# Kernel tuning notes

Measured on AMD Instinct MI355X. Metric: run time of the kernel, lower is better.

Reference implementation:

```python
import jax, jax.numpy as jnp
import numpy as np

NUM_QUBITS = 12
NUM_LAYERS = 4
N_CLASSES = 10
BATCH = 512
BN_EPS = 1e-5


def _apply_1q(state, U, wire):
    """Apply a 1-qubit gate U on `wire`. state: (B,)+(2,)*n; U: (2,2) or (B,2,2)."""
    state = jnp.moveaxis(state, wire + 1, -1)
    if U.ndim == 3:
        out = jnp.einsum('bij,b...j->b...i', U, state)
    else:
        out = jnp.einsum('ij,b...j->b...i', U, state)
    return jnp.moveaxis(out, -1, wire + 1)


def _apply_cnot(state, ctrl, tgt):
    s = jnp.moveaxis(state, (ctrl + 1, tgt + 1), (-2, -1))
    # where control bit == 1, flip the target axis
    s = jnp.concatenate([s[..., 0:1, :], s[..., 1:2, ::-1]], axis=-2)
    return jnp.moveaxis(s, (-2, -1), (ctrl + 1, tgt + 1))


def _rot(phi, theta, omega):
    """PennyLane Rot(phi, theta, omega) = RZ(omega) RY(theta) RZ(phi)."""
    c = jnp.cos(theta / 2)
    s = jnp.sin(theta / 2)
    row0 = jnp.stack([jnp.exp(-1j * (phi + omega) / 2) * c,
                      -jnp.exp(1j * (phi - omega) / 2) * s])
    row1 = jnp.stack([jnp.exp(-1j * (phi - omega) / 2) * s,
                      jnp.exp(1j * (phi + omega) / 2) * c])
    return jnp.stack([row0, row1]).astype(jnp.complex64)


def _circuit(x, weights):
    """Batched state-vector sim of the data-reuploading VQC.
    x: (B, n_qubits) angles; weights: (L, n_qubits, 3). Returns (B, N_CLASSES) <Z_i>."""
    B = x.shape[0]
    state = jnp.zeros((B,) + (2,) * NUM_QUBITS, jnp.complex64)
    state = state.at[(slice(None),) + (0,) * NUM_QUBITS].set(1.0)
    half = (x * 0.5).astype(jnp.float32)
    for l in range(NUM_LAYERS):
        w = weights[l]
        # angle embedding (RY(x_q) on each wire) -- batched gate, differs per sample
        for q in range(NUM_QUBITS):
            c = jnp.cos(half[:, q])
            s = jnp.sin(half[:, q])
            U = jnp.stack([jnp.stack([c, -s], -1),
                           jnp.stack([s, c], -1)], -2).astype(jnp.complex64)  # (B,2,2)
            state = _apply_1q(state, U, q)
        # one StronglyEntangling layer: Rot per wire (shared across batch)
        for q in range(NUM_QUBITS):
            state = _apply_1q(state, _rot(w[q, 0], w[q, 1], w[q, 2]), q)
        # ring of CNOTs (range 1)
        for q in range(NUM_QUBITS):
            state = _apply_cnot(state, q, (q + 1) % NUM_QUBITS)
    probs = jnp.abs(state) ** 2  # (B,)+(2,)*n, float32
    all_axes = tuple(range(1, NUM_QUBITS + 1))
    expz = []
    for i in range(N_CLASSES):
        axes = tuple(a for a in all_axes if a != i + 1)
        p = probs.sum(axis=axes)  # (B, 2) marginal of qubit i
        expz.append(p[:, 0] - p[:, 1])
    return jnp.stack(expz, axis=-1)  # (B, N_CLASSES)


def setup_inputs() -> dict:
    key = jax.random.key(0)
    k1, k2 = jax.random.split(key)
    x = jax.random.normal(k1, (BATCH, NUM_QUBITS), dtype=jnp.float32)
    weights = 0.01 * jax.random.uniform(k2, (NUM_LAYERS, NUM_QUBITS, 3), dtype=jnp.float32)
    bias = jnp.zeros((N_CLASSES,), jnp.float32)
    gamma = jnp.ones((N_CLASSES,), jnp.float32)
    beta = jnp.zeros((N_CLASSES,), jnp.float32)
    return {"x": x, "weights": weights, "bias": bias, "gamma": gamma, "beta": beta}


def reference(x, weights, bias, gamma, beta):
    expz = _circuit(x, weights)
    probs = jax.nn.softmax(expz + bias, axis=-1)
    # BatchNorm1d (training mode): biased batch statistics, affine
    mu = probs.mean(axis=0)
    var = probs.var(axis=0)
    return (probs - mu) / jnp.sqrt(var + BN_EPS) * gamma + beta
```

## Files before the change

kernel.cpp:

```cpp
#include <hip/hip_runtime.h>
#include <math.h>

#define NQ 12
#define NL 4
#define NC 10
#define NB 512
#define BN_EPS 1e-5f

typedef float v2f __attribute__((ext_vector_type(2)));

__device__ __forceinline__ void bfly(v2f& A, v2f& B,
    v2f c0, v2f c1, v2f c2, v2f c3, v2f c4, v2f c5, v2f c6, v2f c7)
{
    const v2f As = A.yx, Bs = B.yx;
    const v2f An = __builtin_elementwise_fma(c0, A,
                   __builtin_elementwise_fma(c1, As,
                   __builtin_elementwise_fma(c2, B, c3 * Bs)));
    const v2f Bn = __builtin_elementwise_fma(c4, A,
                   __builtin_elementwise_fma(c5, As,
                   __builtin_elementwise_fma(c6, B, c7 * Bs)));
    A = An; B = Bn;
}

__global__ __launch_bounds__(512, 4) void vqc_kernel(
    const float* __restrict__ x, const float* __restrict__ w,
    const float* __restrict__ bias, float* __restrict__ probs)
{
    __shared__ v2f buf[2][4096];
    __shared__ __align__(16) float gm[48][16];
    __shared__ float red[8*NC];

    const int b = blockIdx.x;
    const int t = threadIdx.x;

    if (t < 48) {
        const int l = t / NQ, q = t % NQ;
        const float xq = 0.5f * x[b*NQ + q];
        const float cx = cosf(xq), sx = sinf(xq);
        const int wi = (l*NQ + q)*3;
        const float phi = w[wi], tht = w[wi+1], om = w[wi+2];
        const float ct = cosf(0.5f*tht), st = sinf(0.5f*tht);
        const float aa = 0.5f*(phi + om), dd = 0.5f*(phi - om);
        const float ca = cosf(aa), sa = sinf(aa);
        const float cd = cosf(dd), sd = sinf(dd);
        const float u00r =  ca*ct, u00i = -sa*ct;
        const float u01r = -cd*st, u01i = -sd*st;
        const float u10r =  cd*st, u10i = -sd*st;
        const float u11r =  ca*ct, u11i =  sa*ct;
        const float m00r = u00r*cx + u01r*sx, m00i = u00i*cx + u01i*sx;
        const float m01r = u01r*cx - u00r*sx, m01i = u01i*cx - u00i*sx;
        const float m10r = u10r*cx + u11r*sx, m10i = u10i*cx + u11i*sx;
        const float m11r = u11r*cx - u10r*sx, m11i = u11i*cx - u10i*sx;
        float* gp = gm[t];
        gp[0]  =  m00r; gp[1]  = m00r;
        gp[2]  = -m00i; gp[3]  = m00i;
        gp[4]  =  m01r; gp[5]  = m01r;
        gp[6]  = -m01i; gp[7]  = m01i;
        gp[8]  =  m10r; gp[9]  = m10r;
        gp[10] = -m10i; gp[11] = m10i;
        gp[12] =  m11r; gp[13] = m11r;
        gp[14] = -m11i; gp[15] = m11i;
    }
    __syncthreads();

    v2f a[8];
    #pragma unroll
    for (int r = 0; r < 8; ++r) a[r] = (v2f){0.f, 0.f};
    if (t == 0) a[0].x = 1.f;

    const unsigned tu = (unsigned)t;
    const unsigned tw = tu >> 6;
    const unsigned baseB = (tw << 9) | (tu & 63u);
    const unsigned baseC = (tw << 9) | (((tu >> 3) & 7u) << 6) | (tu & 7u);
    const unsigned baseD = (tw << 9) | (((tu >> 3) & 7u) << 6) | ((tu & 7u) << 3);

#define SWZ(i) ((i) ^ (((i) >> 4) & 15u))

    #define STAGE(gbase) \
        _Pragma("unroll") \
        for (int g = 0; g < 3; ++g) { \
            const v2f* cp = (const v2f*)gm[(gbase) + 2 - g]; \
            const v2f c0=cp[0],c1=cp[1],c2=cp[2],c3=cp[3], \
                      c4=cp[4],c5=cp[5],c6=cp[6],c7=cp[7]; \
            const int bit = 1 << g; \
            _Pragma("unroll") \
            for (int r0 = 0; r0 < 8; ++r0) \
                if (!(r0 & bit)) bfly(a[r0], a[r0|bit], c0,c1,c2,c3,c4,c5,c6,c7); \
        }

    #define TRANS(IOLD, INEW) { \
        v2f* bp = buf[pb]; pb ^= 1; \
        _Pragma("unroll") \
        for (int r = 0; r < 8; ++r) { const unsigned i_ = (IOLD); bp[SWZ(i_)] = a[r]; } \
        __syncthreads(); \
        _Pragma("unroll") \
        for (int r = 0; r < 8; ++r) { const unsigned i_ = (INEW); a[r] = bp[SWZ(i_)]; } \
    }

    int pb = 0;
    #pragma unroll
    for (int l = 0; l < NL; ++l) {
        STAGE(l*12)
        TRANS(((unsigned)r << 9) | tu, baseB | ((unsigned)r << 6))
        STAGE(l*12 + 3)
        TRANS(baseB | ((unsigned)r << 6), baseC | ((unsigned)r << 3))
        STAGE(l*12 + 6)
        TRANS(baseC | ((unsigned)r << 3), baseD | (unsigned)r)
        STAGE(l*12 + 9)
        if (l < NL-1) {
            v2f* bp = buf[pb]; pb ^= 1;
            #pragma unroll
            for (int r = 0; r < 8; ++r) {
                unsigned i_ = baseD | (unsigned)r;
                unsigned S = i_ ^ (i_ >> 1);
                S ^= S >> 2; S ^= S >> 4; S ^= S >> 8;
                const unsigned j = S ^ ((S & 1u) << 11);
                bp[SWZ(j)] = a[r];
            }
            __syncthreads();
            #pragma unroll
            for (int r = 0; r < 8; ++r) {
                const unsigned i_ = ((unsigned)r << 9) | tu;
                a[r] = bp[SWZ(i_)];
            }
        }
    }

    const unsigned t8 = (tu >> 8) & 1u;
    const unsigned Q7 = t8 ^ ((tu >> 7) & 1u);
    const unsigned Q6 = Q7 ^ ((tu >> 6) & 1u);
    const unsigned Q5 = Q6 ^ ((tu >> 5) & 1u);
    const unsigned Q4 = Q5 ^ ((tu >> 4) & 1u);
    const unsigned Q3 = Q4 ^ ((tu >> 3) & 1u);
    const unsigned Q2 = Q3 ^ ((tu >> 2) & 1u);
    const unsigned Q1 = Q2 ^ ((tu >> 1) & 1u);
    const unsigned Q0 = Q1 ^ (tu & 1u);

    float psum = 0.f, pflip = 0.f, pflip2 = 0.f;
    #pragma unroll
    for (int r = 0; r < 8; ++r) {
        const float p = a[r].x*a[r].x + a[r].y*a[r].y;
        const int pr = ((r>>2) ^ (r>>1) ^ r) & 1;
        psum  += p;
        pflip  += pr      ? -p : p;
        pflip2 += (r & 4) ? -p : p;
    }
    float acc[NC];
    acc[0] = ((t8 ^ Q0) ? -1.f : 1.f) * pflip;
    acc[1] = (Q7 ? -1.f : 1.f) * psum;
    acc[2] = (Q6 ? -1.f : 1.f) * psum;
    acc[3] = (Q5 ? -1.f : 1.f) * psum;
    acc[4] = (Q4 ? -1.f : 1.f) * psum;
    acc[5] = (Q3 ? -1.f : 1.f) * psum;
    acc[6] = (Q2 ? -1.f : 1.f) * psum;
    acc[7] = (Q1 ? -1.f : 1.f) * psum;
    acc[8] = (Q0 ? -1.f : 1.f) * psum;
    acc[9] = (Q0 ? -1.f : 1.f) * pflip2;

    #pragma unroll
    for (int off = 32; off >= 1; off >>= 1) {
        #pragma unroll
        for (int c = 0; c < NC; ++c)
            acc[c] += __shfl_down(acc[c], off, 64);
    }
    const int wave = t >> 6, lane = t & 63;
    if (lane == 0) {
        #pragma unroll
        for (int c = 0; c < NC; ++c) red[wave*NC + c] = acc[c];
    }
    __syncthreads();
    if (t == 0) {
        float ez[NC];
        float mx = -1e30f;
        #pragma unroll
        for (int c = 0; c < NC; ++c) {
            float s = bias[c];
            #pragma unroll
            for (int wv = 0; wv < 8; ++wv) s += red[wv*NC + c];
            ez[c] = s;
            mx = fmaxf(mx, s);
        }
        float sum = 0.f;
        #pragma unroll
        for (int c = 0; c < NC; ++c) { ez[c] = expf(ez[c] - mx); sum += ez[c]; }
        const float inv = 1.f / sum;
        #pragma unroll
        for (int c = 0; c < NC; ++c) probs[b*NC + c] = ez[c] * inv;
    }
}

__global__ __launch_bounds__(256) void bn_kernel(
    float* __restrict__ probs, const float* __restrict__ gamma,
    const float* __restrict__ beta)
{
    const int c = blockIdx.x;
    const int t = threadIdx.x;
    const float v0 = probs[t*NC + c];
    const float v1 = probs[(t + 256)*NC + c];
    float s  = v0 + v1;
    float ss = v0*v0 + v1*v1;
    #pragma unroll
    for (int off = 32; off >= 1; off >>= 1) {
        s  += __shfl_down(s,  off, 64);
        ss += __shfl_down(ss, off, 64);
    }
    __shared__ float sm[8];
    __shared__ float stat[2];
    const int wave = t >> 6, lane = t & 63;
    if (lane == 0) { sm[wave] = s; sm[4 + wave] = ss; }
    __syncthreads();
    if (t == 0) {
        const float S  = sm[0] + sm[1] + sm[2] + sm[3];
        const float SS = sm[4] + sm[5] + sm[6] + sm[7];
        const float mu  = S * (1.f/512.f);
        const float var = SS * (1.f/512.f) - mu*mu;
        stat[0] = mu;
        stat[1] = 1.f / sqrtf(var + BN_EPS);
    }
    __syncthreads();
    const float mu = stat[0], inv = stat[1];
    const float g = gamma[c], bt = beta[c];
    probs[t*NC + c]         = (v0 - mu) * inv * g + bt;
    probs[(t + 256)*NC + c] = (v1 - mu) * inv * g + bt;
}

extern "C" void kernel_launch(void* const* d_in, const int* in_sizes, int n_in,
                              void* d_out, int out_size, void* d_ws, size_t ws_size,
                              hipStream_t stream) {
    const float* x     = (const float*)d_in[0];
    const float* w     = (const float*)d_in[1];
    const float* bias  = (const float*)d_in[2];
    const float* gamma = (const float*)d_in[3];
    const float* beta  = (const float*)d_in[4];
    float* out = (float*)d_out;

    vqc_kernel<<<NB, 512, 0, stream>>>(x, w, bias, out);
    bn_kernel<<<NC, 256, 0, stream>>>(out, gamma, beta);
}
```

Before: 88.74 us.

## Simulate each sample's state vector in a single wavefront with 64 amplitudes per lane

Each sample is now handled by one 64-thread block instead of eight waves. Every lane holds 64 amplitudes in registers, so six gates are applied locally before each LDS transpose. This leaves two transposes per layer instead of four and removes the cross-wave LDS reduction and its barriers. The cost is heavy register pressure (128 floats of state per lane), less parallelism per sample, and a risk of spills or low occupancy.

```diff
diff --git a/kernel.cpp b/kernel.cpp
--- a/kernel.cpp
+++ b/kernel.cpp
@@ -22,13 +22,12 @@
     A = An; B = Bn;
 }
 
-__global__ __launch_bounds__(512, 4) void vqc_kernel(
+__global__ __launch_bounds__(64) void vqc_kernel(
     const float* __restrict__ x, const float* __restrict__ w,
     const float* __restrict__ bias, float* __restrict__ probs)
 {
-    __shared__ v2f buf[2][4096];
+    __shared__ v2f stg[4096];
     __shared__ __align__(16) float gm[48][16];
-    __shared__ float red[8*NC];
 
     const int b = blockIdx.x;
     const int t = threadIdx.x;
@@ -63,99 +62,90 @@
     }
     __syncthreads();
 
-    v2f a[8];
-    #pragma unroll
-    for (int r = 0; r < 8; ++r) a[r] = (v2f){0.f, 0.f};
+    const unsigned lane = (unsigned)t;
+    const unsigned l0=lane&1u, l1=(lane>>1)&1u, l2=(lane>>2)&1u,
+                   l3=(lane>>3)&1u, l4=(lane>>4)&1u, l5=(lane>>5)&1u;
+    const unsigned S5=l5, S4=S5^l4, S3=S4^l3, S2=S3^l2, S1=S2^l1, S0=S1^l0;
+    const unsigned Hbase = ((S5^S0)<<5)|(S4<<4)|(S3<<3)|(S2<<2)|(S1<<1)|S0;
+    const unsigned Gt    = S3 | (S2<<1) | (S1<<2);
+    const unsigned maskP = S0 ? 63u : 0u;
+    const unsigned baseW = (Hbase<<6) | (maskP ^ Gt);
+    const unsigned lane65 = lane * 65u;
+
+    v2f a[64];
+    #pragma unroll
+    for (int r = 0; r < 64; ++r) a[r] = (v2f){0.f, 0.f};
     if (t == 0) a[0].x = 1.f;
 
-    const unsigned tu = (unsigned)t;
-    const unsigned tw = tu >> 6;
-    const unsigned baseB = (tw << 9) | (tu & 63u);
-    const unsigned baseC = (tw << 9) | (((tu >> 3) & 7u) << 6) | (tu & 7u);
-    const unsigned baseD = (tw << 9) | (((tu >> 3) & 7u) << 6) | ((tu & 7u) << 3);
-
-#define SWZ(i) ((i) ^ (((i) >> 4) & 15u))
-
-    #define STAGE(gbase) \
+    #define GATEK(row, kbit) { \
+        const v2f* cp = (const v2f*)gm[row]; \
+        const v2f c0=cp[0],c1=cp[1],c2=cp[2],c3=cp[3], \
+                  c4=cp[4],c5=cp[5],c6=cp[6],c7=cp[7]; \
         _Pragma("unroll") \
-        for (int g = 0; g < 3; ++g) { \
-            const v2f* cp = (const v2f*)gm[(gbase) + 2 - g]; \
-            const v2f c0=cp[0],c1=cp[1],c2=cp[2],c3=cp[3], \
-                      c4=cp[4],c5=cp[5],c6=cp[6],c7=cp[7]; \
-            const int bit = 1 << g; \
-            _Pragma("unroll") \
-            for (int r0 = 0; r0 < 8; ++r0) \
-                if (!(r0 & bit)) bfly(a[r0], a[r0|bit], c0,c1,c2,c3,c4,c5,c6,c7); \
-        }
-
-    #define TRANS(IOLD, INEW) { \
-        v2f* bp = buf[pb]; pb ^= 1; \
-        _Pragma("unroll") \
-        for (int r = 0; r < 8; ++r) { const unsigned i_ = (IOLD); bp[SWZ(i_)] = a[r]; } \
-        __syncthreads(); \
-        _Pragma("unroll") \
-        for (int r = 0; r < 8; ++r) { const unsigned i_ = (INEW); a[r] = bp[SWZ(i_)]; } \
-    }
-
-    int pb = 0;
-    #pragma unroll
+        for (int r0 = 0; r0 < 64; ++r0) \
+            if (!(r0 & (kbit))) bfly(a[r0], a[r0|(kbit)], c0,c1,c2,c3,c4,c5,c6,c7); \
+    }
+
+    #pragma unroll 1
     for (int l = 0; l < NL; ++l) {
-        STAGE(l*12)
-        TRANS(((unsigned)r << 9) | tu, baseB | ((unsigned)r << 6))
-        STAGE(l*12 + 3)
-        TRANS(baseB | ((unsigned)r << 6), baseC | ((unsigned)r << 3))
-        STAGE(l*12 + 6)
-        TRANS(baseC | ((unsigned)r << 3), baseD | (unsigned)r)
-        STAGE(l*12 + 9)
+        const int g0 = l*12;
+        #pragma unroll
+        for (int k = 0; k < 6; ++k) GATEK(g0 + 5 - k, 1<<k)
+
+        __syncthreads();
+        #pragma unroll
+        for (int r = 0; r < 64; ++r) stg[lane ^ (unsigned)(65*r)] = a[r];
+        __syncthreads();
+        #pragma unroll
+        for (int r = 0; r < 64; ++r) a[r] = stg[lane65 ^ (unsigned)r];
+
+        #pragma unroll
+        for (int k = 0; k < 6; ++k) GATEK(g0 + 11 - k, 1<<k)
+
         if (l < NL-1) {
-            v2f* bp = buf[pb]; pb ^= 1;
+            __syncthreads();
             #pragma unroll
-            for (int r = 0; r < 8; ++r) {
-                unsigned i_ = baseD | (unsigned)r;
-                unsigned S = i_ ^ (i_ >> 1);
-                S ^= S >> 2; S ^= S >> 4; S ^= S >> 8;
-                const unsigned j = S ^ ((S & 1u) << 11);
-                bp[SWZ(j)] = a[r];
+            for (int r = 0; r < 64; ++r) {
+                const unsigned r5=((unsigned)r>>5)&1u, r4=((unsigned)r>>4)&1u,
+                               r3=((unsigned)r>>3)&1u, r2=((unsigned)r>>2)&1u,
+                               r1=((unsigned)r>>1)&1u, r0b=(unsigned)r&1u;
+                const unsigned SR5=r5, SR4=SR5^r4, SR3=SR4^r3,
+                               SR2=SR3^r2, SR1=SR2^r1, SR0=SR1^r0b;
+                const unsigned SRval = SR0|(SR1<<1)|(SR2<<2)|(SR3<<3)|(SR4<<4)|(SR5<<5);
+                stg[baseW ^ ((SR0<<11) ^ SRval)] = a[r];
             }
             __syncthreads();
             #pragma unroll
-            for (int r = 0; r < 8; ++r) {
-                const unsigned i_ = ((unsigned)r << 9) | tu;
-                a[r] = bp[SWZ(i_)];
+            for (int r = 0; r < 64; ++r) {
+                const unsigned gp = (((unsigned)r>>3)&1u)
+                                  | ((((unsigned)r>>2)&1u)<<1)
+                                  | ((((unsigned)r>>1)&1u)<<2);
+                a[r] = stg[lane ^ (((unsigned)r<<6) | gp)];
             }
         }
     }
 
-    const unsigned t8 = (tu >> 8) & 1u;
-    const unsigned Q7 = t8 ^ ((tu >> 7) & 1u);
-    const unsigned Q6 = Q7 ^ ((tu >> 6) & 1u);
-    const unsigned Q5 = Q6 ^ ((tu >> 5) & 1u);
-    const unsigned Q4 = Q5 ^ ((tu >> 4) & 1u);
-    const unsigned Q3 = Q4 ^ ((tu >> 3) & 1u);
-    const unsigned Q2 = Q3 ^ ((tu >> 2) & 1u);
-    const unsigned Q1 = Q2 ^ ((tu >> 1) & 1u);
-    const unsigned Q0 = Q1 ^ (tu & 1u);
-
-    float psum = 0.f, pflip = 0.f, pflip2 = 0.f;
-    #pragma unroll
-    for (int r = 0; r < 8; ++r) {
+    float psum=0.f, fP=0.f, f5=0.f, f4=0.f, f3=0.f, f2=0.f;
+    #pragma unroll
+    for (int r = 0; r < 64; ++r) {
         const float p = a[r].x*a[r].x + a[r].y*a[r].y;
-        const int pr = ((r>>2) ^ (r>>1) ^ r) & 1;
-        psum  += p;
-        pflip  += pr      ? -p : p;
-        pflip2 += (r & 4) ? -p : p;
-    }
+        const unsigned r5=((unsigned)r>>5)&1u, r4=((unsigned)r>>4)&1u,
+                       r3=((unsigned)r>>3)&1u, r2=((unsigned)r>>2)&1u,
+                       r1=((unsigned)r>>1)&1u, r0b=(unsigned)r&1u;
+        const unsigned sr4=r4^r5, sr3=r3^sr4, sr2=r2^sr3, pr=sr2^r1^r0b;
+        psum += p;
+        fP += pr  ? -p : p;
+        f5 += r5  ? -p : p;
+        f4 += sr4 ? -p : p;
+        f3 += sr3 ? -p : p;
+        f2 += sr2 ? -p : p;
+    }
+    const float sA0=(S5^S0)?-1.f:1.f, sq1=S4?-1.f:1.f, sq2=S3?-1.f:1.f,
+                sq3=S2?-1.f:1.f, sq4=S1?-1.f:1.f, sq5=S0?-1.f:1.f;
     float acc[NC];
-    acc[0] = ((t8 ^ Q0) ? -1.f : 1.f) * pflip;
-    acc[1] = (Q7 ? -1.f : 1.f) * psum;
-    acc[2] = (Q6 ? -1.f : 1.f) * psum;
-    acc[3] = (Q5 ? -1.f : 1.f) * psum;
-    acc[4] = (Q4 ? -1.f : 1.f) * psum;
-    acc[5] = (Q3 ? -1.f : 1.f) * psum;
-    acc[6] = (Q2 ? -1.f : 1.f) * psum;
-    acc[7] = (Q1 ? -1.f : 1.f) * psum;
-    acc[8] = (Q0 ? -1.f : 1.f) * psum;
-    acc[9] = (Q0 ? -1.f : 1.f) * pflip2;
+    acc[0]=sA0*fP;   acc[1]=sq1*psum; acc[2]=sq2*psum; acc[3]=sq3*psum;
+    acc[4]=sq4*psum; acc[5]=sq5*psum; acc[6]=sq5*f5;   acc[7]=sq5*f4;
+    acc[8]=sq5*f3;   acc[9]=sq5*f2;
 
     #pragma unroll
     for (int off = 32; off >= 1; off >>= 1) {
@@ -163,22 +153,13 @@
         for (int c = 0; c < NC; ++c)
             acc[c] += __shfl_down(acc[c], off, 64);
     }
-    const int wave = t >> 6, lane = t & 63;
-    if (lane == 0) {
-        #pragma unroll
-        for (int c = 0; c < NC; ++c) red[wave*NC + c] = acc[c];
-    }
-    __syncthreads();
     if (t == 0) {
         float ez[NC];
         float mx = -1e30f;
         #pragma unroll
         for (int c = 0; c < NC; ++c) {
-            float s = bias[c];
-            #pragma unroll
-            for (int wv = 0; wv < 8; ++wv) s += red[wv*NC + c];
-            ez[c] = s;
-            mx = fmaxf(mx, s);
+            ez[c] = acc[c] + bias[c];
+            mx = fmaxf(mx, ez[c]);
         }
         float sum = 0.f;
         #pragma unroll
@@ -234,6 +215,6 @@
     const float* beta  = (const float*)d_in[4];
     float* out = (float*)d_out;
 
-    vqc_kernel<<<NB, 512, 0, stream>>>(x, w, bias, out);
+    vqc_kernel<<<NB, 64, 0, stream>>>(x, w, bias, out);
     bn_kernel<<<NC, 256, 0, stream>>>(out, gamma, beta);
 }
```

New measurement: 108.5 us. 1.22x slower.
